# Kernel optimization log

Hardware: AMD Instinct MI355X
Metric: run time of the kernel (lower is better)

## Reference

```python
import jax, jax.numpy as jnp
import numpy as np

N_NODES = 100000


def setup_inputs() -> dict:
    key = jax.random.key(0)
    k1, k2, k3, k4, k5 = jax.random.split(key, 5)
    features = jax.random.normal(k1, (N_NODES, 512), dtype=jnp.float32)
    edge_src = jax.random.randint(k2, (640000,), 0, N_NODES, dtype=jnp.int64)
    edge_dst = jax.random.randint(k3, (640000,), 0, N_NODES, dtype=jnp.int64)
    edge_weight = jax.random.uniform(k4, (640000,), dtype=jnp.float32)
    weights = jax.random.normal(k5, (512, 128), dtype=jnp.float32) * (2.0 / 512) ** 0.5  # kaiming-ish scale
    bias = jnp.zeros((128,), dtype=jnp.float32)
    return {
        "features": features,
        "edge_src": edge_src,
        "edge_dst": edge_dst,
        "edge_weight": edge_weight,
        "weights": weights,
        "bias": bias,
    }


def reference(features, edge_src, edge_dst, edge_weight, weights, bias):
    # X' = A @ (X @ W) + b, with sparse A given as COO edges (src -> dst).
    h = jnp.matmul(features, weights)                      # [N, d_out] dense GEMM
    msg = edge_weight[:, None] * h[edge_src]               # [E, d_out] gather + scale
    out = jax.ops.segment_sum(msg, edge_dst, num_segments=N_NODES)  # sparse aggregation
    return out + bias
```

## Files before the change

### kernel.cpp

```cpp
#include <hip/hip_runtime.h>


#define D_IN  512
#define D_OUT 128
#define CAP   32

typedef __attribute__((ext_vector_type(8))) short short8;
typedef __attribute__((ext_vector_type(4))) float f32x4;
typedef __attribute__((ext_vector_type(4))) int i32x4;
typedef __attribute__((ext_vector_type(8))) unsigned short u16x8;
typedef __attribute__((ext_vector_type(2))) unsigned long long u64x2;

typedef __attribute__((address_space(1))) const unsigned int glob_u32;
typedef __attribute__((address_space(3))) unsigned int lds_u32;

static __device__ __forceinline__ unsigned short f2bf(float f) {
    unsigned u = __float_as_uint(f);
    unsigned r = (u + 0x7FFFu + ((u >> 16) & 1u)) >> 16;
    return (unsigned short)r;
}

static __device__ __forceinline__ int pack2(float lo, float hi) {
    return (int)((__float_as_uint(hi) & 0xFFFF0000u) | (__float_as_uint(lo) >> 16));
}

__global__ __launch_bounds__(256) void prep_kernel(const float* __restrict__ W,
                                                   unsigned short* __restrict__ Wt,
                                                   int* __restrict__ deg,
                                                   unsigned long long* __restrict__ bucket,
                                                   int M) {
    int t = blockIdx.x * 256 + threadIdx.x;
    if (t < D_OUT * D_IN) {
        int n = t >> 9;
        int k = t & 511;
        Wt[t] = f2bf(W[(size_t)k * D_OUT + n]);
    }
    if (t < M) deg[t] = 0;
    const int stride = gridDim.x * 256;
    const int npair = M * (CAP / 2);
    u64x2 z = {0ull, 0ull};
    for (int i = t; i < npair; i += stride)
        __builtin_nontemporal_store(z, reinterpret_cast<u64x2*>(bucket) + i);
}

__global__ __launch_bounds__(256, 3) void gemm_build_kernel(
        const float* __restrict__ X, const unsigned short* __restrict__ Wt,
        unsigned short* __restrict__ H, int M,
        const int* __restrict__ src, const int* __restrict__ dst,
        const float* __restrict__ w, int* __restrict__ deg,
        unsigned long long* __restrict__ bucket, int E, int nG) {
    __shared__ float As[2 * 128 * 32];
    __shared__ unsigned short Bs[2 * 128 * 32];

    if ((int)blockIdx.x >= nG) {
        int e = ((int)blockIdx.x - nG) * 256 + threadIdx.x;
        if (e < E) {
            int d = dst[e];
            int pos = atomicAdd(&deg[d], 1);
            if (pos < CAP)
                bucket[(size_t)d * CAP + pos] =
                    ((unsigned long long)__float_as_uint(w[e]) << 32) | (unsigned)src[e];
        }
        return;
    }

    const int tid = threadIdx.x;
    const int lane = tid & 63;
    const int wv = tid >> 6;
    const int block_row = blockIdx.x * 128;

    const int m = lane & 15;
    const int q = lane >> 4;
    const int wave_row = (wv >> 1) * 64;
    const int wave_col = (wv & 1) * 64;

    f32x4 acc[4][4];
#pragma unroll
    for (int a = 0; a < 4; a++)
#pragma unroll
        for (int b = 0; b < 4; b++) acc[a][b] = (f32x4){0.f, 0.f, 0.f, 0.f};

#define STAGE(BUF, T)                                                          \
    do {                                                                       \
        const int kc_ = (T) * 32;                                              \
        _Pragma("unroll") for (int it = 0; it < 4; it++) {                     \
            int slot_base = wv * 256 + it * 64;              \
            int s = slot_base + lane;                                          \
            int row = s >> 3;                                                  \
            int kq = (s & 7) ^ (row & 7);                                      \
            int grow = block_row + row;                                        \
            if (grow >= M) grow = M - 1;                                       \
            const float* gp = X + (size_t)grow * D_IN + kc_ + kq * 4;          \
            __builtin_amdgcn_global_load_lds((glob_u32*)gp,                    \
                (lds_u32*)(As + (BUF) * 4096 + (size_t)slot_base * 4), 16, 0, 0); \
        }                                                                      \
        _Pragma("unroll") for (int it = 0; it < 2; it++) {                     \
            int slot_base = wv * 128 + it * 64;                                \
            int s = slot_base + lane;                                          \
            int n = s >> 2;                                                    \
            int kq = (s & 3) ^ (n & 3);                                        \
            const unsigned short* gp = Wt + (size_t)n * D_IN + kc_ + kq * 8;   \
            __builtin_amdgcn_global_load_lds((glob_u32*)gp,                    \
                (lds_u32*)(Bs + (BUF) * 4096 + (size_t)slot_base * 8), 16, 0, 0); \
        }                                                                      \
    } while (0)

#define COMPUTE(BUF)                                                           \
    do {                                                                       \
        const float* Ap = As + (BUF) * 4096;                                   \
        const unsigned short* Bp = Bs + (BUF) * 4096;                          \
        short8 afr[4];                                                         \
        _Pragma("unroll") for (int rg = 0; rg < 4; rg++) {                     \
            int row = wave_row + rg * 16 + m;                                  \
            int kq0 = 2 * q;                                                   \
            f32x4 u0 = *reinterpret_cast<const f32x4*>(                        \
                Ap + (size_t)(row * 8 + (kq0 ^ (row & 7))) * 4);               \
            f32x4 u1 = *reinterpret_cast<const f32x4*>(                        \
                Ap + (size_t)(row * 8 + ((kq0 + 1) ^ (row & 7))) * 4);         \
            i32x4 ai;                                                          \
            ai.x = pack2(u0.x, u0.y);                                          \
            ai.y = pack2(u0.z, u0.w);                                          \
            ai.z = pack2(u1.x, u1.y);                                          \
            ai.w = pack2(u1.z, u1.w);                                          \
            afr[rg] = __builtin_bit_cast(short8, ai);                          \
        }                                                                      \
        short8 bfr[4];                                                         \
        _Pragma("unroll") for (int cg = 0; cg < 4; cg++) {                     \
            int n = wave_col + cg * 16 + m;                                    \
            bfr[cg] = *reinterpret_cast<const short8*>(                        \
                Bp + (size_t)(n * 4 + (q ^ (n & 3))) * 8);                     \
        }                                                                      \
        _Pragma("unroll") for (int rg = 0; rg < 4; rg++)                       \
            _Pragma("unroll") for (int cg = 0; cg < 4; cg++)                   \
                acc[rg][cg] = __builtin_amdgcn_mfma_f32_16x16x32_bf16(         \
                    afr[rg], bfr[cg], acc[rg][cg], 0, 0, 0);                   \
    } while (0)

#define STEP(BUF, T, VMS)                                                      \
    do {                                                                       \
        if ((T) + 1 < 16) STAGE((BUF) ^ 1, (T) + 1);                           \
        asm volatile("s_waitcnt vmcnt(" VMS ")" ::: "memory");                 \
        __builtin_amdgcn_s_barrier();                                          \
        asm volatile("" ::: "memory");     \
        COMPUTE(BUF);                                                          \
        __builtin_amdgcn_s_barrier();                                          \
        asm volatile("" ::: "memory");                                         \
    } while (0)

    STAGE(0, 0);
    STEP(0, 0, "6");
    STEP(1, 1, "6");
    STEP(0, 2, "6");
    STEP(1, 3, "6");
    STEP(0, 4, "6");
    STEP(1, 5, "6");
    STEP(0, 6, "6");
    STEP(1, 7, "6");
    STEP(0, 8, "6");
    STEP(1, 9, "6");
    STEP(0, 10, "6");
    STEP(1, 11, "6");
    STEP(0, 12, "6");
    STEP(1, 13, "6");
    STEP(0, 14, "6");
    STEP(1, 15, "0");

#undef STAGE
#undef COMPUTE
#undef STEP

#pragma unroll
    for (int rg = 0; rg < 4; rg++) {
#pragma unroll
        for (int r = 0; r < 4; r++) {
            int grow = block_row + wave_row + rg * 16 + q * 4 + r;
            if (grow < M) {
#pragma unroll
                for (int cg = 0; cg < 4; cg++)
                    H[(size_t)grow * D_OUT + wave_col + cg * 16 + m] = f2bf(acc[rg][cg][r]);
            }
        }
    }
}

__global__ __launch_bounds__(256) void agg_kernel(const unsigned short* __restrict__ H,
                                                  const int* __restrict__ deg,
                                                  const unsigned long long* __restrict__ bucket,
                                                  const float* __restrict__ bias,
                                                  float* __restrict__ out, int M) {
    int row = blockIdx.x * 16 + (threadIdx.x >> 4);
    if (row >= M) return;
    int sub = threadIdx.x & 15;

    f32x4 b0 = *reinterpret_cast<const f32x4*>(bias + sub * 8);
    f32x4 b1 = *reinterpret_cast<const f32x4*>(bias + sub * 8 + 4);
    float acc[8] = {b0.x, b0.y, b0.z, b0.w, b1.x, b1.y, b1.z, b1.w};

    int n = deg[row];
    if (n > CAP) n = CAP;
    const unsigned long long* bp = bucket + (size_t)row * CAP;

    for (int j = 0; j < n; j += 8) {
        u64x2 q0 = __builtin_nontemporal_load(reinterpret_cast<const u64x2*>(bp + j));
        u64x2 q1 = __builtin_nontemporal_load(reinterpret_cast<const u64x2*>(bp + j + 2));
        u64x2 q2 = __builtin_nontemporal_load(reinterpret_cast<const u64x2*>(bp + j + 4));
        u64x2 q3 = __builtin_nontemporal_load(reinterpret_cast<const u64x2*>(bp + j + 6));
        unsigned long long p[8] = {q0[0], q0[1], q1[0], q1[1], q2[0], q2[1], q3[0], q3[1]};
        u16x8 v[8];
#pragma unroll
        for (int i = 0; i < 8; i++)
            v[i] = *reinterpret_cast<const u16x8*>(
                H + (size_t)(unsigned)(p[i] & 0xFFFFFFFFull) * D_OUT + sub * 8);
#pragma unroll
        for (int i = 0; i < 8; i++) {
            float wi = __uint_as_float((unsigned)(p[i] >> 32));
#pragma unroll
            for (int c = 0; c < 8; c++)
                acc[c] += wi * __uint_as_float((unsigned)v[i][c] << 16);
        }
    }

    f32x4 o0 = {acc[0], acc[1], acc[2], acc[3]};
    f32x4 o1 = {acc[4], acc[5], acc[6], acc[7]};
    __builtin_nontemporal_store(o0, reinterpret_cast<f32x4*>(out + (size_t)row * D_OUT + sub * 8));
    __builtin_nontemporal_store(o1, reinterpret_cast<f32x4*>(out + (size_t)row * D_OUT + sub * 8 + 4));
}

extern "C" void kernel_launch(void* const* d_in, const int* in_sizes, int n_in,
                              void* d_out, int out_size, void* d_ws, size_t ws_size,
                              hipStream_t stream) {
    const float* features    = (const float*)d_in[0];
    const int*   edge_src    = (const int*)d_in[1];
    const int*   edge_dst    = (const int*)d_in[2];
    const float* edge_weight = (const float*)d_in[3];
    const float* weights     = (const float*)d_in[4];
    const float* bias        = (const float*)d_in[5];
    float* out = (float*)d_out;

    const int M = in_sizes[0] / D_IN;
    const int E = in_sizes[1];

    char* ws = (char*)d_ws;
    unsigned short* hbf = (unsigned short*)(ws);
    unsigned short* Wt  = (unsigned short*)(ws + 25600000);
    int* deg            = (int*)(ws + 25731072);
    unsigned long long* bucket = (unsigned long long*)(ws + 26131456);

    int mx = (M > D_OUT * D_IN) ? M : (D_OUT * D_IN);
    prep_kernel<<<(mx + 255) / 256, 256, 0, stream>>>(weights, Wt, deg, bucket, M);

    const int nG = (M + 127) / 128;
    const int nB = (E + 255) / 256;
    gemm_build_kernel<<<nG + nB, 256, 0, stream>>>(features, Wt, hbf, M,
                                                   edge_src, edge_dst, edge_weight,
                                                   deg, bucket, E, nG);

    agg_kernel<<<(M + 15) / 16, 256, 0, stream>>>(hbf, deg, bucket, bias, out, M);
}
```

Measured before the change: 380.6 us.

## Split edge bucketing from GEMM, pad degree counters, skip bucket zeroing

Moves the edge-bucketing atomics out of the fused GEMM launch into a separate build kernel that runs before the GEMM. Each degree counter is padded to its own 128-byte slot so atomics on different rows do not share a cache line. Only the padded counters are zeroed now, not the whole bucket array. In exchange, the aggregation kernel masks weights and clamps indices for slots past the degree. The cost is one extra launch and losing the overlap between the atomics and the GEMM.

```diff
diff --git a/kernel.cpp b/kernel.cpp
--- a/kernel.cpp
+++ b/kernel.cpp
@@ -4,6 +4,7 @@
 #define D_IN  512
 #define D_OUT 128
 #define CAP   32
+#define DEGS  32
 
 typedef __attribute__((ext_vector_type(8))) short short8;
 typedef __attribute__((ext_vector_type(4))) float f32x4;
@@ -26,43 +27,42 @@
 
 __global__ __launch_bounds__(256) void prep_kernel(const float* __restrict__ W,
                                                    unsigned short* __restrict__ Wt,
-                                                   int* __restrict__ deg,
-                                                   unsigned long long* __restrict__ bucket,
-                                                   int M) {
+                                                   int* __restrict__ deg2, int M) {
     int t = blockIdx.x * 256 + threadIdx.x;
     if (t < D_OUT * D_IN) {
         int n = t >> 9;
         int k = t & 511;
         Wt[t] = f2bf(W[(size_t)k * D_OUT + n]);
     }
-    if (t < M) deg[t] = 0;
     const int stride = gridDim.x * 256;
-    const int npair = M * (CAP / 2);
+    const int nvec = M * 8;
     u64x2 z = {0ull, 0ull};
-    for (int i = t; i < npair; i += stride)
-        __builtin_nontemporal_store(z, reinterpret_cast<u64x2*>(bucket) + i);
-}
-
-__global__ __launch_bounds__(256, 3) void gemm_build_kernel(
-        const float* __restrict__ X, const unsigned short* __restrict__ Wt,
-        unsigned short* __restrict__ H, int M,
-        const int* __restrict__ src, const int* __restrict__ dst,
-        const float* __restrict__ w, int* __restrict__ deg,
-        unsigned long long* __restrict__ bucket, int E, int nG) {
+    for (int i = t; i < nvec; i += stride)
+        __builtin_nontemporal_store(z, reinterpret_cast<u64x2*>(deg2) + i);
+}
+
+__global__ __launch_bounds__(256) void build_kernel(const int* __restrict__ src,
+                                                    const int* __restrict__ dst,
+                                                    const float* __restrict__ w,
+                                                    int* __restrict__ deg2,
+                                                    unsigned long long* __restrict__ bucket,
+                                                    int E) {
+    int e = blockIdx.x * 256 + threadIdx.x;
+    if (e >= E) return;
+    int d = dst[e];
+    int pos = atomicAdd(&deg2[(size_t)d * DEGS], 1);
+    if (pos < CAP) {
+        unsigned long long v =
+            ((unsigned long long)__float_as_uint(w[e]) << 32) | (unsigned)src[e];
+        __builtin_nontemporal_store(v, bucket + (size_t)d * CAP + pos);
+    }
+}
+
+__global__ __launch_bounds__(256, 3) void gemm_kernel(const float* __restrict__ X,
+                                                      const unsigned short* __restrict__ Wt,
+                                                      unsigned short* __restrict__ H, int M) {
     __shared__ float As[2 * 128 * 32];
     __shared__ unsigned short Bs[2 * 128 * 32];
-
-    if ((int)blockIdx.x >= nG) {
-        int e = ((int)blockIdx.x - nG) * 256 + threadIdx.x;
-        if (e < E) {
-            int d = dst[e];
-            int pos = atomicAdd(&deg[d], 1);
-            if (pos < CAP)
-                bucket[(size_t)d * CAP + pos] =
-                    ((unsigned long long)__float_as_uint(w[e]) << 32) | (unsigned)src[e];
-        }
-        return;
-    }
 
     const int tid = threadIdx.x;
     const int lane = tid & 63;
@@ -141,7 +141,7 @@
         if ((T) + 1 < 16) STAGE((BUF) ^ 1, (T) + 1);                           \
         asm volatile("s_waitcnt vmcnt(" VMS ")" ::: "memory");                 \
         __builtin_amdgcn_s_barrier();                                          \
-        asm volatile("" ::: "memory");     \
+        asm volatile("" ::: "memory");                                         \
         COMPUTE(BUF);                                                          \
         __builtin_amdgcn_s_barrier();                                          \
         asm volatile("" ::: "memory");                                         \
@@ -184,7 +184,7 @@
 }
 
 __global__ __launch_bounds__(256) void agg_kernel(const unsigned short* __restrict__ H,
-                                                  const int* __restrict__ deg,
+                                                  const int* __restrict__ deg2,
                                                   const unsigned long long* __restrict__ bucket,
                                                   const float* __restrict__ bias,
                                                   float* __restrict__ out, int M) {
@@ -196,7 +196,7 @@
     f32x4 b1 = *reinterpret_cast<const f32x4*>(bias + sub * 8 + 4);
     float acc[8] = {b0.x, b0.y, b0.z, b0.w, b1.x, b1.y, b1.z, b1.w};
 
-    int n = deg[row];
+    int n = deg2[(size_t)row * DEGS];
     if (n > CAP) n = CAP;
     const unsigned long long* bp = bucket + (size_t)row * CAP;
 
@@ -207,16 +207,19 @@
         u64x2 q3 = __builtin_nontemporal_load(reinterpret_cast<const u64x2*>(bp + j + 6));
         unsigned long long p[8] = {q0[0], q0[1], q1[0], q1[1], q2[0], q2[1], q3[0], q3[1]};
         u16x8 v[8];
-#pragma unroll
-        for (int i = 0; i < 8; i++)
-            v[i] = *reinterpret_cast<const u16x8*>(
-                H + (size_t)(unsigned)(p[i] & 0xFFFFFFFFull) * D_OUT + sub * 8);
+        float wgt[8];
 #pragma unroll
         for (int i = 0; i < 8; i++) {
-            float wi = __uint_as_float((unsigned)(p[i] >> 32));
+            unsigned idx = (unsigned)(p[i] & 0xFFFFFFFFull);
+            if (idx >= (unsigned)M) idx = 0;
+            v[i] = *reinterpret_cast<const u16x8*>(H + (size_t)idx * D_OUT + sub * 8);
+            wgt[i] = (j + i < n) ? __uint_as_float((unsigned)(p[i] >> 32)) : 0.0f;
+        }
+#pragma unroll
+        for (int i = 0; i < 8; i++) {
 #pragma unroll
             for (int c = 0; c < 8; c++)
-                acc[c] += wi * __uint_as_float((unsigned)v[i][c] << 16);
+                acc[c] += wgt[i] * __uint_as_float((unsigned)v[i][c] << 16);
         }
     }
 
@@ -243,17 +246,12 @@
     char* ws = (char*)d_ws;
     unsigned short* hbf = (unsigned short*)(ws);
     unsigned short* Wt  = (unsigned short*)(ws + 25600000);
-    int* deg            = (int*)(ws + 25731072);
-    unsigned long long* bucket = (unsigned long long*)(ws + 26131456);
-
-    int mx = (M > D_OUT * D_IN) ? M : (D_OUT * D_IN);
-    prep_kernel<<<(mx + 255) / 256, 256, 0, stream>>>(weights, Wt, deg, bucket, M);
-
-    const int nG = (M + 127) / 128;
-    const int nB = (E + 255) / 256;
-    gemm_build_kernel<<<nG + nB, 256, 0, stream>>>(features, Wt, hbf, M,
-                                                   edge_src, edge_dst, edge_weight,
-                                                   deg, bucket, E, nG);
-
-    agg_kernel<<<(M + 15) / 16, 256, 0, stream>>>(hbf, deg, bucket, bias, out, M);
-}
+    int* deg2           = (int*)(ws + 25731072);
+    unsigned long long* bucket = (unsigned long long*)(ws + 38531328);
+
+    prep_kernel<<<(M + 255) / 256, 256, 0, stream>>>(weights, Wt, deg2, M);
+    build_kernel<<<(E + 255) / 256, 256, 0, stream>>>(edge_src, edge_dst, edge_weight,
+                                                      deg2, bucket, E);
+    gemm_kernel<<<(M + 127) / 128, 256, 0, stream>>>(features, Wt, hbf, M);
+    agg_kernel<<<(M + 15) / 16, 256, 0, stream>>>(hbf, deg2, bucket, bias, out, M);
+}
```

Measured after the change: 413.3 us. 8.6% more time.
